# Kernel optimization log

Hardware: AMD Instinct MI355X
Metric: run time of the kernel (lower is better)

Reference implementation:

```python
import jax, jax.numpy as jnp
import numpy as np
from jax import lax

G = 1000  # hard-coded grid size in ConvCNP.forward
LOG_2PI = float(np.log(2.0 * np.pi))


def _conv1d(x, w, b):
    # x: (B, Cin, L), w: (Cout, Cin, K), SAME padding, stride 1 (k=5, pad=2)
    y = lax.conv_general_dilated(x, w, (1,), 'SAME',
                                 dimension_numbers=('NCH', 'OIH', 'NCH'))
    return y + b[None, :, None]


def setup_inputs() -> dict:
    key = jax.random.key(0)
    ks = jax.random.split(key, 16)
    B, Nc, Nt = 32, 2048, 2048
    inp = {
        'x_context': jax.random.normal(ks[0], (B, 1, Nc), jnp.float32),
        'y_context': jax.random.normal(ks[1], (B, 1, Nc), jnp.float32),
        'x_target': jax.random.normal(ks[2], (B, 1, Nt), jnp.float32),
        'y_target': jax.random.normal(ks[3], (B, 1, Nt), jnp.float32),
        # learned kernel lengthscales (nn.Parameter init 0.5)
        'ls_x': jnp.asarray(0.5, jnp.float32),
        'ls_rho': jnp.asarray(0.5, jnp.float32),
        # SimpleCNN(2, 1): channels [2, 16, 32, 16, 2], k=5
        'W1': 0.1 * jax.random.normal(ks[4], (16, 2, 5), jnp.float32),
        'b1': jnp.zeros((16,), jnp.float32),
        'W2': 0.1 * jax.random.normal(ks[5], (32, 16, 5), jnp.float32),
        'b2': jnp.zeros((32,), jnp.float32),
        'W3': 0.1 * jax.random.normal(ks[6], (16, 32, 5), jnp.float32),
        'b3': jnp.zeros((16,), jnp.float32),
        'W4': 0.1 * jax.random.normal(ks[7], (2, 16, 5), jnp.float32),
        'b4': jnp.zeros((2,), jnp.float32),
    }
    return inp


def _forward(x_context, y_context, x_target, y_target,
             ls_x, ls_rho, W1, b1, W2, b2, W3, b3, W4, b4):
    B = x_context.shape[0]
    xc = x_context[:, 0, :]            # (B, Nc)
    xt = x_target[:, 0, :]             # (B, Nt)
    t = jnp.linspace(-2.2, 2.2, G).astype(x_context.dtype)  # (G,)

    # phi(y) = [1, y] density/signal channels: (B, 2, Nc)
    phi = jnp.concatenate([jnp.ones_like(y_context), y_context], axis=1)

    # EQ-kernel interpolation context -> grid: w[b,g,n] = exp(-(t_g-x_n)^2/(2 l^2))
    d2 = (t[None, :, None] - xc[:, None, :]) ** 2           # (B, G, Nc)
    w_x = jnp.exp(-d2 / (2.0 * ls_x * ls_x))
    h = jnp.einsum('bgn,bcn->bcg', w_x, phi)                # (B, 2, G)

    density = h[:, 0:1, :]
    rest = h[:, 1:, :] / (density + 1e-8)
    h = jnp.concatenate([density, rest], axis=1)            # (B, 2, G)

    # SimpleCNN
    y = jax.nn.relu(_conv1d(h, W1, b1))
    y = jax.nn.relu(_conv1d(y, W2, b2))
    y = jax.nn.relu(_conv1d(y, W3, b3))
    y = _conv1d(y, W4, b4)                                  # (B, 2, G)
    y_mu_grid = y[:, 0:1, :]
    y_sigma_grid = jax.nn.softplus(y[:, 1:2, :])
    y_grid = jnp.concatenate([y_mu_grid, y_sigma_grid], axis=1)  # (B, 2, G)

    # EQ-kernel interpolation grid -> targets
    d2t = (xt[:, :, None] - t[None, None, :]) ** 2          # (B, Nt, G)
    w_rho = jnp.exp(-d2t / (2.0 * ls_rho * ls_rho))
    y_pred = jnp.einsum('btg,bcg->bct', w_rho, y_grid)      # (B, 2, Nt)

    mu = y_pred[:, 0:1, :]
    sigma = y_pred[:, 1:2, :]

    # Normal(mu, sigma).log_prob(y_target), mean over points, sum over batch
    z = (y_target - mu) / sigma
    logp = -0.5 * z * z - jnp.log(sigma) - 0.5 * LOG_2PI    # (B, 1, Nt)
    loss = -jnp.sum(jnp.mean(logp, axis=-1))
    return mu.transpose(0, 2, 1), sigma.transpose(0, 2, 1), loss


def reference(x_context, y_context, x_target, y_target,
              ls_x, ls_rho, W1, b1, W2, b2, W3, b3, W4, b4):
    return _forward(x_context, y_context, x_target, y_target,
                    ls_x, ls_rho, W1, b1, W2, b2, W3, b3, W4, b4)
```

## Files before the change

kernel.cpp:

```cpp
#include <hip/hip_runtime.h>
#include <math.h>

#define G     1000
#define B     32
#define NC    2048
#define NT    2048
#define BN    (B * NT)
#define LOG2E 1.4426950408889634f
#define LN2PI 1.8378770664093453f

#if __has_builtin(__builtin_amdgcn_exp2f)
#define EXP2F(x) __builtin_amdgcn_exp2f(x)
#else
#define EXP2F(x) exp2f(x)
#endif

__global__ __launch_bounds__(512) void k_smooth(
    const float* __restrict__ xc, const float* __restrict__ yc,
    const float* __restrict__ ls_x, float* __restrict__ h,
    float* __restrict__ loss_slot) {
  __shared__ float sxy[NC * 2];
  __shared__ float pA0[512], pA1[512], pB0[512], pB1[512];
  if (blockIdx.x == 0 && blockIdx.y == 0 && threadIdx.x == 0) *loss_slot = 0.f;

  int tid = threadIdx.x;
  int b = blockIdx.y, tile = blockIdx.x;
  float ls = ls_x[0];
  float s  = sqrtf(0.5f * LOG2E) / ls;

  const float* xb = xc + b * NC;
  const float* yb = yc + b * NC;
  for (int n = tid; n < NC; n += 512) {
    sxy[2 * n]     = s * xb[n];
    sxy[2 * n + 1] = yb[n];
  }
  __syncthreads();

  int lane = tid & 63, wv = tid >> 6;
  int ga = tile * 128 + lane;
  float step = s * (4.4f / 999.f);
  float tga = s * -2.2f + step * (float)ga;
  float tgb = tga + step * 64.f;

  float a0 = 0.f, a1 = 0.f, b0 = 0.f, b1 = 0.f;
  const float4* p = ((const float4*)sxy) + wv * (NC / 16);
  #pragma unroll 4
  for (int i = 0; i < NC / 16; ++i) {
    float4 v = p[i];
    float d, w;
    d = tga - v.x; w = EXP2F(-(d * d)); a0 += w; a1 = fmaf(w, v.y, a1);
    d = tgb - v.x; w = EXP2F(-(d * d)); b0 += w; b1 = fmaf(w, v.y, b1);
    d = tga - v.z; w = EXP2F(-(d * d)); a0 += w; a1 = fmaf(w, v.w, a1);
    d = tgb - v.z; w = EXP2F(-(d * d)); b0 += w; b1 = fmaf(w, v.w, b1);
  }
  pA0[tid] = a0; pA1[tid] = a1; pB0[tid] = b0; pB1[tid] = b1;
  __syncthreads();

  if (tid < 128) {
    int which = tid >> 6, l = tid & 63;
    int g = tile * 128 + which * 64 + l;
    if (g < G) {
      const float* q0 = which ? pB0 : pA0;
      const float* q1 = which ? pB1 : pA1;
      float d0 = 0.f, d1 = 0.f;
      #pragma unroll
      for (int k = 0; k < 8; ++k) { d0 += q0[l + 64 * k]; d1 += q1[l + 64 * k]; }
      h[(b * 2 + 0) * G + g] = d0;
      h[(b * 2 + 1) * G + g] = d1 / (d0 + 1e-8f);
    }
  }
}

#define TILE  48
#define NTILE 21
#define CSTR  68

template <int CIN, int COUT, int S4>
__device__ __forceinline__ void conv8(
    const float* __restrict__ in, float* __restrict__ out,
    const float4* __restrict__ wf4, const float* __restrict__ w4p,
    const float* __restrict__ bias, int tid) {
  if (tid < COUT * 8) {
    int oc = tid % COUT;
    int i0 = (tid / COUT) * 8;
    float acc[8];
    float bb = bias[oc];
    #pragma unroll
    for (int p = 0; p < 8; ++p) acc[p] = bb;
    for (int ic = 0; ic < CIN; ++ic) {
      const float4* ip = (const float4*)(in + ic * CSTR + i0);
      float4 A = ip[0], Bv = ip[1], C = ip[2];
      float v[12] = {A.x, A.y, A.z, A.w, Bv.x, Bv.y, Bv.z, Bv.w, C.x, C.y, C.z, C.w};
      float4 w = wf4[oc * S4 + ic];
      float w4v = w4p[ic * COUT + oc];
      #pragma unroll
      for (int p = 0; p < 8; ++p)
        acc[p] = fmaf(v[p], w.x, fmaf(v[p+1], w.y, fmaf(v[p+2], w.z,
                 fmaf(v[p+3], w.w, fmaf(v[p+4], w4v, acc[p])))));
    }
    float* op = out + oc * CSTR + i0 + 2;
    #pragma unroll
    for (int j = 0; j < 4; ++j)
      *(float2*)(op + 2 * j) = make_float2(fmaxf(acc[2*j], 0.f), fmaxf(acc[2*j+1], 0.f));
  }
}

__global__ __launch_bounds__(256, 2) void k_conv(
    const float* __restrict__ h,
    const float* __restrict__ W1, const float* __restrict__ Bs1,
    const float* __restrict__ W2, const float* __restrict__ Bs2,
    const float* __restrict__ W3, const float* __restrict__ Bs3,
    const float* __restrict__ W4, const float* __restrict__ Bs4,
    float* __restrict__ yg) {
  __shared__ __align__(16) float bufA[32 * CSTR], bufB[32 * CSTR];
  __shared__ float4 wf1[16 * 3], wf2[32 * 17], wf3[16 * 33];
  __shared__ float  w41[2 * 16], w42[16 * 32], w43[32 * 16];
  __shared__ float  wt4[162];
  __shared__ float  sB1[16], sB2[32], sB3[16], sB4[2];

  int tid  = threadIdx.x;
  int tile = blockIdx.x, b = blockIdx.y;
  int ts   = tile * TILE;

  if (tid < 32) {
    int oc = tid >> 1, ic = tid & 1, a = oc * 10 + ic * 5;
    wf1[oc * 3 + ic] = make_float4(W1[a], W1[a+1], W1[a+2], W1[a+3]);
    w41[ic * 16 + oc] = W1[a + 4];
  }
  for (int pr = tid; pr < 512; pr += 256) {
    int oc = pr >> 4, ic = pr & 15, a = oc * 80 + ic * 5;
    wf2[oc * 17 + ic] = make_float4(W2[a], W2[a+1], W2[a+2], W2[a+3]);
    w42[ic * 32 + oc] = W2[a + 4];
  }
  for (int pr = tid; pr < 512; pr += 256) {
    int oc = pr >> 5, ic = pr & 31, a = oc * 160 + ic * 5;
    wf3[oc * 33 + ic] = make_float4(W3[a], W3[a+1], W3[a+2], W3[a+3]);
    w43[ic * 16 + oc] = W3[a + 4];
  }
  for (int i = tid; i < 160; i += 256) wt4[(i / 80) * 81 + i % 80] = W4[i];
  if (tid < 16)       sB1[tid]      = Bs1[tid];
  else if (tid < 48)  sB2[tid - 16] = Bs2[tid - 16];
  else if (tid < 64)  sB3[tid - 48] = Bs3[tid - 48];
  else if (tid < 66)  sB4[tid - 64] = Bs4[tid - 64];

  for (int i = tid; i < 2 * CSTR; i += 256) {
    int c = i >= CSTR, col = i - c * CSTR;
    int g = ts + col - 10;
    bufA[c * CSTR + col] = (g >= 0 && g < G) ? h[(b * 2 + c) * G + g] : 0.f;
  }
  __syncthreads();

  conv8<2, 16, 3>(bufA, bufB, wf1, w41, sB1, tid);
  __syncthreads();
  conv8<16, 32, 17>(bufB, bufA, wf2, w42, sB2, tid);
  __syncthreads();
  conv8<32, 16, 33>(bufA, bufB, wf3, w43, sB3, tid);
  __syncthreads();

  if (tid < 96) {
    int oc = tid >= 48;
    int j  = tid - oc * 48;
    int i  = 10 + j;
    float sacc = sB4[oc];
    #pragma unroll
    for (int ic = 0; ic < 16; ++ic) {
      const float* ip = bufB + ic * CSTR + i - 2;
      #pragma unroll
      for (int k = 0; k < 5; ++k)
        sacc = fmaf(ip[k], wt4[oc * 81 + ic * 5 + k], sacc);
    }
    int gp = ts + j;
    if (gp < G) {
      if (oc == 0) {
        yg[(b * 2 + 0) * G + gp] = sacc;
      } else {
        float sp_ = fmaxf(sacc, 0.f) + log1pf(__expf(-fabsf(sacc)));
        yg[(b * 2 + 1) * G + gp] = sp_;
      }
    }
  }
}

__global__ __launch_bounds__(512) void k_pred(
    const float* __restrict__ xt, const float* __restrict__ yt,
    const float* __restrict__ ls_rho, const float* __restrict__ yg,
    float* __restrict__ out) {
  __shared__ float4 sp[512];
  __shared__ float pA0[512], pA1[512], pB0[512], pB1[512];
  __shared__ float red[8];

  int tid = threadIdx.x;
  int b = blockIdx.y, tile = blockIdx.x;
  float ls = ls_rho[0];
  float s  = sqrtf(0.5f * LOG2E) / ls;
  float dl = s * (4.4f / 999.f);

  const float* y0 = yg + (b * 2 + 0) * G;
  const float* y1 = yg + (b * 2 + 1) * G;
  {
    int g0 = 2 * tid, g1 = 2 * tid + 1;
    float a0 = (g0 < G) ? y0[g0] : 0.f, b0_ = (g0 < G) ? y1[g0] : 0.f;
    float a1 = (g1 < G) ? y0[g1] : 0.f, b1_ = (g1 < G) ? y1[g1] : 0.f;
    sp[tid] = make_float4(a0, b0_, a1, b1_);
  }
  __syncthreads();

  int lane = tid & 63, wv = tid >> 6;
  int ta = tile * 128 + lane;
  float ua = s * xt[b * NT + ta];
  float ub = s * xt[b * NT + ta + 64];
  float base = 2.2f * s - dl * (float)(wv * 128);
  float aa = ua + base, ab = ub + base;
  float Wa = EXP2F(64.f - aa * aa), qa = EXP2F(dl * (aa + aa) - dl * dl);
  float Wb = EXP2F(64.f - ab * ab), qb = EXP2F(dl * (ab + ab) - dl * dl);
  float r  = EXP2F(-2.f * dl * dl);

  float muA = 0.f, sgA = 0.f, muB = 0.f, sgB = 0.f;
  const float4* p = sp + wv * 64;
  #pragma unroll 4
  for (int i = 0; i < 64; ++i) {
    float4 v = p[i];
    muA = fmaf(Wa, v.x, muA); sgA = fmaf(Wa, v.y, sgA); Wa *= qa; qa *= r;
    muB = fmaf(Wb, v.x, muB); sgB = fmaf(Wb, v.y, sgB); Wb *= qb; qb *= r;
    muA = fmaf(Wa, v.z, muA); sgA = fmaf(Wa, v.w, sgA); Wa *= qa; qa *= r;
    muB = fmaf(Wb, v.z, muB); sgB = fmaf(Wb, v.w, sgB); Wb *= qb; qb *= r;
  }
  pA0[tid] = muA; pA1[tid] = sgA; pB0[tid] = muB; pB1[tid] = sgB;
  __syncthreads();

  float lp = 0.f;
  if (tid < 128) {
    int which = tid >> 6, l = tid & 63;
    int t = tile * 128 + which * 64 + l;
    const float* q0 = which ? pB0 : pA0;
    const float* q1 = which ? pB1 : pA1;
    float mu = 0.f, sg = 0.f;
    #pragma unroll
    for (int k = 0; k < 8; ++k) { mu += q0[l + 64 * k]; sg += q1[l + 64 * k]; }
    mu *= 0x1p-64f;
    sg *= 0x1p-64f;
    out[b * NT + t]      = mu;
    out[BN + b * NT + t] = sg;
    float z = (yt[b * NT + t] - mu) / sg;
    lp = -0.5f * z * z - __logf(sg) - 0.5f * LN2PI;
  }
  #pragma unroll
  for (int m = 32; m; m >>= 1) lp += __shfl_xor(lp, m);
  if ((tid & 63) == 0) red[tid >> 6] = lp;
  __syncthreads();
  if (tid == 0) {
    float tot = 0.f;
    #pragma unroll
    for (int i = 0; i < 8; ++i) tot += red[i];
    atomicAdd(out + 2 * BN, -tot * (1.f / (float)NT));
  }
}

extern "C" void kernel_launch(void* const* d_in, const int* in_sizes, int n_in,
                              void* d_out, int out_size, void* d_ws, size_t ws_size,
                              hipStream_t stream) {
  const float* xc  = (const float*)d_in[0];
  const float* yc  = (const float*)d_in[1];
  const float* xt  = (const float*)d_in[2];
  const float* yt  = (const float*)d_in[3];
  const float* lsx = (const float*)d_in[4];
  const float* lsr = (const float*)d_in[5];
  const float* W1  = (const float*)d_in[6];  const float* b1 = (const float*)d_in[7];
  const float* W2  = (const float*)d_in[8];  const float* b2 = (const float*)d_in[9];
  const float* W3  = (const float*)d_in[10]; const float* b3 = (const float*)d_in[11];
  const float* W4  = (const float*)d_in[12]; const float* b4 = (const float*)d_in[13];

  float* out = (float*)d_out;
  float* h   = (float*)d_ws;
  float* yg  = h + B * 2 * G;

  k_smooth<<<dim3(8, B), 512, 0, stream>>>(xc, yc, lsx, h, out + 2 * BN);
  k_conv<<<dim3(NTILE, B), 256, 0, stream>>>(h, W1, b1, W2, b2, W3, b3, W4, b4, yg);
  k_pred<<<dim3(16, B), 512, 0, stream>>>(xt, yt, lsr, yg, out);
}
```

Measured before the change: 43.92 us.

## Replace per-pair exp in context smoothing with geometric recurrence over grid points

Result: faster. 42.31 us (-3.6%).

```diff
diff --git a/kernel.cpp b/kernel.cpp
--- a/kernel.cpp
+++ b/kernel.cpp
@@ -19,52 +19,68 @@
     const float* __restrict__ xc, const float* __restrict__ yc,
     const float* __restrict__ ls_x, float* __restrict__ h,
     float* __restrict__ loss_slot) {
-  __shared__ float sxy[NC * 2];
-  __shared__ float pA0[512], pA1[512], pB0[512], pB1[512];
+  __shared__ float2 sxy[NC];
+  __shared__ float2 part[8][128];
   if (blockIdx.x == 0 && blockIdx.y == 0 && threadIdx.x == 0) *loss_slot = 0.f;
 
   int tid = threadIdx.x;
   int b = blockIdx.y, tile = blockIdx.x;
-  float ls = ls_x[0];
-  float s  = sqrtf(0.5f * LOG2E) / ls;
+  float ls  = ls_x[0];
+  float s   = sqrtf(0.5f * LOG2E) / ls;
+  float dlt = s * (4.4f / 999.f);
 
   const float* xb = xc + b * NC;
   const float* yb = yc + b * NC;
-  for (int n = tid; n < NC; n += 512) {
-    sxy[2 * n]     = s * xb[n];
-    sxy[2 * n + 1] = yb[n];
-  }
-  __syncthreads();
-
-  int lane = tid & 63, wv = tid >> 6;
-  int ga = tile * 128 + lane;
-  float step = s * (4.4f / 999.f);
-  float tga = s * -2.2f + step * (float)ga;
-  float tgb = tga + step * 64.f;
-
-  float a0 = 0.f, a1 = 0.f, b0 = 0.f, b1 = 0.f;
-  const float4* p = ((const float4*)sxy) + wv * (NC / 16);
+  for (int n = tid; n < NC; n += 512) sxy[n] = make_float2(s * xb[n], yb[n]);
+  __syncthreads();
+
+  int lane = tid & 63, w = tid >> 6;
+  int ns = lane & 7, gr = lane >> 3;
+  int g0 = tile * 128 + gr * 16;
+  float v0 = s * -2.2f + dlt * (float)g0;
+  float r  = EXP2F(-2.f * dlt * dlt);
+
+  float h0[16], h1[16];
+  #pragma unroll
+  for (int j = 0; j < 16; ++j) { h0[j] = 0.f; h1[j] = 0.f; }
+
+  const float2* base = sxy + w * 256 + ns;
   #pragma unroll 4
-  for (int i = 0; i < NC / 16; ++i) {
-    float4 v = p[i];
-    float d, w;
-    d = tga - v.x; w = EXP2F(-(d * d)); a0 += w; a1 = fmaf(w, v.y, a1);
-    d = tgb - v.x; w = EXP2F(-(d * d)); b0 += w; b1 = fmaf(w, v.y, b1);
-    d = tga - v.z; w = EXP2F(-(d * d)); a0 += w; a1 = fmaf(w, v.w, a1);
-    d = tgb - v.z; w = EXP2F(-(d * d)); b0 += w; b1 = fmaf(w, v.w, b1);
-  }
-  pA0[tid] = a0; pA1[tid] = a1; pB0[tid] = b0; pB1[tid] = b1;
+  for (int i = 0; i < 32; ++i) {
+    float2 v = base[i * 8];
+    float a = v.x - v0;
+    float W = EXP2F(64.f - a * a);
+    float q = EXP2F(fmaf(2.f * dlt, a, -dlt * dlt));
+    #pragma unroll
+    for (int j = 0; j < 16; ++j) {
+      h0[j] += W;
+      h1[j] = fmaf(W, v.y, h1[j]);
+      W *= q; q *= r;
+    }
+  }
+  #pragma unroll
+  for (int m = 1; m < 8; m <<= 1) {
+    #pragma unroll
+    for (int j = 0; j < 16; ++j) {
+      h0[j] += __shfl_xor(h0[j], m);
+      h1[j] += __shfl_xor(h1[j], m);
+    }
+  }
+  {
+    int j0 = ns * 2;
+    part[w][gr * 16 + j0]     = make_float2(h0[j0], h1[j0]);
+    part[w][gr * 16 + j0 + 1] = make_float2(h0[j0 + 1], h1[j0 + 1]);
+  }
   __syncthreads();
 
   if (tid < 128) {
-    int which = tid >> 6, l = tid & 63;
-    int g = tile * 128 + which * 64 + l;
+    int g = tile * 128 + tid;
     if (g < G) {
-      const float* q0 = which ? pB0 : pA0;
-      const float* q1 = which ? pB1 : pA1;
       float d0 = 0.f, d1 = 0.f;
       #pragma unroll
-      for (int k = 0; k < 8; ++k) { d0 += q0[l + 64 * k]; d1 += q1[l + 64 * k]; }
+      for (int k = 0; k < 8; ++k) { float2 pv = part[k][tid]; d0 += pv.x; d1 += pv.y; }
+      d0 *= 0x1p-64f;
+      d1 *= 0x1p-64f;
       h[(b * 2 + 0) * G + g] = d0;
       h[(b * 2 + 1) * G + g] = d1 / (d0 + 1e-8f);
     }
```
